# Kernel tuning notes

Hardware: AMD Instinct MI355X
Metric: run time of the kernel (lower is better)

The kernel has to match this reference:

```python
import jax, jax.numpy as jnp
import numpy as np

N = 20000
E = 640000


def setup_inputs() -> dict:
    key = jax.random.key(0)
    k1, k2, k3, k4 = jax.random.split(key, 4)
    IN, H, C = 4096, 512, 10
    x = jax.random.normal(k1, (N, IN), dtype=jnp.float32)
    edge_index = jax.random.randint(k2, (2, E), 0, N, dtype=jnp.int64)
    W1 = jax.random.normal(k3, (IN, H), dtype=jnp.float32) * (1.0 / np.sqrt(IN))
    b1 = jnp.zeros((H,), dtype=jnp.float32)
    W2 = jax.random.normal(k4, (H, C), dtype=jnp.float32) * (1.0 / np.sqrt(H))
    b2 = jnp.zeros((C,), dtype=jnp.float32)
    return {"x": x, "edge_index": edge_index, "W1": W1, "b1": b1, "W2": W2, "b2": b2}


def _gcn_conv(x, src, dst, W, b):
    # Dense transform first (PyG GCNConv does XW then propagate).
    h = x @ W  # [N, F_out]
    # Add self loops.
    loops = jnp.arange(N, dtype=src.dtype)
    s = jnp.concatenate([src, loops])
    d = jnp.concatenate([dst, loops])
    # Symmetric normalization D^{-1/2} (A+I) D^{-1/2}; degree counted on dst.
    deg = jax.ops.segment_sum(jnp.ones_like(d, dtype=h.dtype), d, num_segments=N)
    dinv = jnp.where(deg > 0, jax.lax.rsqrt(deg), 0.0)
    norm = dinv[s] * dinv[d]  # [E+N]
    msg = h[s] * norm[:, None]  # gather + scale
    out = jax.ops.segment_sum(msg, d, num_segments=N)  # scatter-add aggregate
    return out + b


def reference(x, edge_index, W1, b1, W2, b2):
    src, dst = edge_index[0], edge_index[1]
    h = _gcn_conv(x, src, dst, W1, b1)  # conv1 (dropout disabled / eval)
    h = jax.nn.relu(h)
    h = _gcn_conv(h, src, dst, W2, b2)  # conv2
    return jax.nn.log_softmax(h, axis=1)
```

## Files before the change

kernel.cpp:

```cpp
#include <hip/hip_runtime.h>
#include <cstdint>
#include <cstddef>

#define NN  20000
#define EE  640000
#define KIN 4096
#define HD  512
#define NC  10
#define CAP 128

typedef __attribute__((ext_vector_type(8))) short short8;
typedef __attribute__((ext_vector_type(4))) float f32x4;

__device__ __forceinline__ unsigned short f2b(float f) {
  union { float f; unsigned int u; } v; v.f = f;
  unsigned int r = v.u + 0x7fffu + ((v.u >> 16) & 1u);
  return (unsigned short)(r >> 16);
}

__device__ __forceinline__ void gload16(const void* g, void* l) {
  __builtin_amdgcn_global_load_lds(
      (const __attribute__((address_space(1))) unsigned int*)g,
      (__attribute__((address_space(3))) unsigned int*)l, 16, 0, 0);
}

__global__ __launch_bounds__(256) void scatk(const int* __restrict__ src, const int* __restrict__ dst,
                                             int* __restrict__ deg, int* __restrict__ csr) {
  int e = blockIdx.x * 256 + threadIdx.x;
  if (e < EE) {
    int d = dst[e];
    int p = atomicAdd(&deg[d], 1);
    csr[d * CAP + p] = src[e];
  }
}

__global__ __launch_bounds__(256) void dinvk(const int* __restrict__ deg, float* __restrict__ dinv) {
  int i = blockIdx.x * 256 + threadIdx.x;
  if (i < NN) dinv[i] = 1.0f / sqrtf((float)(deg[i] + 1));
}

__global__ __launch_bounds__(256) void transk(const float* __restrict__ W1, unsigned short* __restrict__ w1t) {
  __shared__ float tile[32][33];
  int h0 = blockIdx.x * 32;
  int k0 = blockIdx.y * 32;
  int tx = threadIdx.x & 31, ty = threadIdx.x >> 5;
#pragma unroll
  for (int r = 0; r < 4; ++r) {
    int k = ty * 4 + r;
    tile[k][tx] = W1[(size_t)(k0 + k) * HD + h0 + tx];
  }
  __syncthreads();
#pragma unroll
  for (int r = 0; r < 4; ++r) {
    int h = ty * 4 + r;
    w1t[(size_t)(h0 + h) * KIN + k0 + tx] = f2b(tile[tx][h]);
  }
}

__global__ __launch_bounds__(256) void gemm1(const float* __restrict__ x,
                                             const unsigned short* __restrict__ w1t,
                                             unsigned short* __restrict__ h1b) {
  __shared__ __align__(16) unsigned short As[64 * 64];
  __shared__ __align__(16) unsigned short Bs[128 * 64];
  int t = threadIdx.x;
  int l = t & 63, w = t >> 6;
  int wm = w >> 1, wn = w & 1;
  int bm = (int)(blockIdx.x >> 2) * 64;
  int bn = (int)(blockIdx.x & 3) * 128;

  int stRow = t >> 3;
  int stQ = (t & 7) ^ (stRow & 7);
  const float* ga[2];
#pragma unroll
  for (int i = 0; i < 2; ++i) {
    int m = bm + i * 32 + stRow;
    if (m > NN - 1) m = NN - 1;
    ga[i] = x + (size_t)m * KIN + stQ * 8;
  }

  int rl = l >> 3;
  int cq = (l & 7) ^ rl;
  const unsigned short* gb[4];
  unsigned short* lB[4];
#pragma unroll
  for (int i = 0; i < 4; ++i) {
    int rowB = bn + i * 32 + w * 8 + rl;
    gb[i] = w1t + (size_t)rowB * KIN + cq * 8;
    lB[i] = Bs + (i * 32 + w * 8) * 64;
  }

  int col0 = ((l >> 4) ^ (l & 7));
  int fm[2], fn[4];
#pragma unroll
  for (int i = 0; i < 2; ++i) fm[i] = (wm * 32 + i * 16 + (l & 15)) * 64 + col0 * 8;
#pragma unroll
  for (int j = 0; j < 4; ++j) fn[j] = (wn * 64 + j * 16 + (l & 15)) * 64 + col0 * 8;

  f32x4 acc[2][4] = {};

  for (int kt = 0; kt < KIN / 64; ++kt) {
    int k0 = kt * 64;
    __syncthreads();
#pragma unroll
    for (int i = 0; i < 4; ++i) gload16(gb[i] + k0, lB[i]);
#pragma unroll
    for (int i = 0; i < 2; ++i) {
      float4 a0 = *reinterpret_cast<const float4*>(ga[i] + k0);
      float4 a1 = *reinterpret_cast<const float4*>(ga[i] + k0 + 4);
      uint4 val;
      val.x = (unsigned int)f2b(a0.x) | ((unsigned int)f2b(a0.y) << 16);
      val.y = (unsigned int)f2b(a0.z) | ((unsigned int)f2b(a0.w) << 16);
      val.z = (unsigned int)f2b(a1.x) | ((unsigned int)f2b(a1.y) << 16);
      val.w = (unsigned int)f2b(a1.z) | ((unsigned int)f2b(a1.w) << 16);
      *reinterpret_cast<uint4*>(As + i * 2048 + 8 * t) = val;
    }
    __syncthreads();
#pragma unroll
    for (int kk = 0; kk < 2; ++kk) {
      int xr = kk << 5;
      short8 af[2], bf[4];
#pragma unroll
      for (int i = 0; i < 2; ++i) af[i] = *reinterpret_cast<const short8*>(As + (fm[i] ^ xr));
#pragma unroll
      for (int j = 0; j < 4; ++j) bf[j] = *reinterpret_cast<const short8*>(Bs + (fn[j] ^ xr));
#pragma unroll
      for (int i = 0; i < 2; ++i)
#pragma unroll
        for (int j = 0; j < 4; ++j)
          acc[i][j] = __builtin_amdgcn_mfma_f32_16x16x32_bf16(af[i], bf[j], acc[i][j], 0, 0, 0);
    }
  }

  int lq = l >> 4;
  bool even = (l & 1) == 0;
#pragma unroll
  for (int i = 0; i < 2; ++i) {
    int row0 = bm + wm * 32 + i * 16 + lq * 4;
#pragma unroll
    for (int j = 0; j < 4; ++j) {
      int col = bn + wn * 64 + j * 16 + (l & 15);
#pragma unroll
      for (int r = 0; r < 4; ++r) {
        float v0 = acc[i][j][r];
        float v1 = __shfl_xor(v0, 1);
        int row = row0 + r;
        if (even && row < NN) {
          unsigned int pk = (unsigned int)f2b(v0) | ((unsigned int)f2b(v1) << 16);
          *reinterpret_cast<unsigned int*>(h1b + (size_t)row * HD + col) = pk;
        }
      }
    }
  }
}

__global__ __launch_bounds__(256) void sgk(const unsigned short* __restrict__ h1b, const int* __restrict__ deg,
                                           const int* __restrict__ csr, const float* __restrict__ dinv,
                                           const float* __restrict__ b1, const float* __restrict__ W2,
                                           float* __restrict__ h2) {
  __shared__ int s_idx[CAP];
  __shared__ float s_w[CAP];
  __shared__ float red[4][NC];
  int i = blockIdx.x;
  int c = threadIdx.x;
  float di = dinv[i];
  int dg = deg[i];
  if (c < dg) {
    int s = csr[i * CAP + c];
    s_idx[c] = s;
    s_w[c] = dinv[s] * di;
  }
  const unsigned int* h1v = reinterpret_cast<const unsigned int*>(h1b);
  unsigned int su = h1v[(size_t)i * 256 + c];
  float wself = di * di;
  float a0 = __uint_as_float(su << 16) * wself;
  float a1 = __uint_as_float(su & 0xffff0000u) * wself;
  __syncthreads();
#pragma unroll 4
  for (int jj = 0; jj < dg; ++jj) {
    unsigned int u = h1v[(size_t)s_idx[jj] * 256 + c];
    float wgt = s_w[jj];
    a0 += __uint_as_float(u << 16) * wgt;
    a1 += __uint_as_float(u & 0xffff0000u) * wgt;
  }
  float2 bb = reinterpret_cast<const float2*>(b1)[c];
  float zx = fmaxf(a0 + bb.x, 0.f);
  float zy = fmaxf(a1 + bb.y, 0.f);
  const float* w2r = W2 + (size_t)(2 * c) * NC;
  float part[NC];
#pragma unroll
  for (int cc = 0; cc < NC; ++cc) part[cc] = zx * w2r[cc] + zy * w2r[NC + cc];
#pragma unroll
  for (int cc = 0; cc < NC; ++cc) {
#pragma unroll
    for (int m = 1; m < 64; m <<= 1) part[cc] += __shfl_xor(part[cc], m, 64);
  }
  int wv = c >> 6, ln = c & 63;
  if (ln == 0) {
#pragma unroll
    for (int cc = 0; cc < NC; ++cc) red[wv][cc] = part[cc];
  }
  __syncthreads();
  if (c < NC) h2[(size_t)i * NC + c] = red[0][c] + red[1][c] + red[2][c] + red[3][c];
}

__global__ __launch_bounds__(64) void spmm2(const float* __restrict__ h2, const int* __restrict__ deg,
                                            const int* __restrict__ csr, const float* __restrict__ dinv,
                                            const float* __restrict__ b2, float* __restrict__ out) {
  int i = blockIdx.x;
  int l = threadIdx.x;
  float di = dinv[i];
  int dg = deg[i];
  float acc[NC] = {};
  for (int e = l; e < dg; e += 64) {
    int s = csr[i * CAP + e];
    float wgt = dinv[s] * di;
    const float2* hp = reinterpret_cast<const float2*>(h2 + (size_t)s * NC);
#pragma unroll
    for (int cc = 0; cc < 5; ++cc) {
      float2 v = hp[cc];
      acc[2 * cc] += v.x * wgt;
      acc[2 * cc + 1] += v.y * wgt;
    }
  }
  if (l == 0) {
    float ws = di * di;
#pragma unroll
    for (int cc = 0; cc < NC; ++cc) acc[cc] += h2[(size_t)i * NC + cc] * ws;
  }
#pragma unroll
  for (int cc = 0; cc < NC; ++cc) {
#pragma unroll
    for (int m = 1; m < 64; m <<= 1) acc[cc] += __shfl_xor(acc[cc], m, 64);
  }
  if (l == 0) {
    float v[NC];
    float mx = -1e30f;
#pragma unroll
    for (int cc = 0; cc < NC; ++cc) {
      v[cc] = acc[cc] + b2[cc];
      mx = fmaxf(mx, v[cc]);
    }
    float s = 0.f;
#pragma unroll
    for (int cc = 0; cc < NC; ++cc) s += expf(v[cc] - mx);
    float lse = mx + logf(s);
#pragma unroll
    for (int cc = 0; cc < NC; ++cc) out[(size_t)i * NC + cc] = v[cc] - lse;
  }
}

extern "C" void kernel_launch(void* const* d_in, const int* in_sizes, int n_in,
                              void* d_out, int out_size, void* d_ws, size_t ws_size,
                              hipStream_t stream) {
  (void)in_sizes; (void)n_in; (void)out_size; (void)ws_size;
  const float* x  = (const float*)d_in[0];
  const int*   ei = (const int*)d_in[1];
  const float* W1 = (const float*)d_in[2];
  const float* b1 = (const float*)d_in[3];
  const float* W2 = (const float*)d_in[4];
  const float* b2 = (const float*)d_in[5];
  float* out = (float*)d_out;
  char* ws = (char*)d_ws;

  unsigned short* w1t = (unsigned short*)(ws);
  unsigned short* h1b = (unsigned short*)(ws + 4194304);
  float* h2   = (float*)(ws + 24674304);
  int*   deg  = (int*)(ws + 25474304);
  float* dinv = (float*)(ws + 25554304);
  int*   csr  = (int*)(ws + 25634304);

  const int* srcp = ei;
  const int* dstp = ei + EE;

  hipMemsetAsync(deg, 0, NN * sizeof(int), stream);
  scatk<<<(EE + 255) / 256, 256, 0, stream>>>(srcp, dstp, deg, csr);
  dinvk<<<(NN + 255) / 256, 256, 0, stream>>>(deg, dinv);
  transk<<<dim3(16, 128), 256, 0, stream>>>(W1, w1t);
  gemm1<<<313 * 4, 256, 0, stream>>>(x, w1t, h1b);
  sgk<<<NN, 256, 0, stream>>>(h1b, deg, csr, dinv, b1, W2, h2);
  spmm2<<<NN, 64, 0, stream>>>(h2, deg, csr, dinv, b2, out);
}
```

Baseline: 740.3 us.

## Remap GEMM blocks across XCDs, use packed bf16 convert, widen aggregation loads

Three separate changes. gemm1 block indices are remapped so each group of 8 interleaved blocks covers a contiguous range of tiles. The aim is for neighbouring tiles to land on the same XCD and share L2 for the x rows and W1 columns; the grid is padded to 1256 blocks so it divides by 8. The software bf16 rounding is replaced with the hardware v_cvt_pk_bf16_f32 instruction. The sgk aggregation kernel now uses 128 threads that each gather 4 bf16 features with a uint2 load, which halves the thread count and the wave-reduction partials. The risks are the changed tile order, lower occupancy per block in sgk, and possible NaN-handling differences in the conversion.

```diff
diff --git a/kernel.cpp b/kernel.cpp
--- a/kernel.cpp
+++ b/kernel.cpp
@@ -18,11 +18,20 @@
   return (unsigned short)(r >> 16);
 }
 
+__device__ __forceinline__ unsigned int cvt2(float lo, float hi) {
+  unsigned int r;
+  asm("v_cvt_pk_bf16_f32 %0, %1, %2" : "=v"(r) : "v"(lo), "v"(hi));
+  return r;
+}
+
 __device__ __forceinline__ void gload16(const void* g, void* l) {
   __builtin_amdgcn_global_load_lds(
       (const __attribute__((address_space(1))) unsigned int*)g,
       (__attribute__((address_space(3))) unsigned int*)l, 16, 0, 0);
 }
+
+__device__ __forceinline__ float bflo(unsigned int u) { return __uint_as_float(u << 16); }
+__device__ __forceinline__ float bfhi(unsigned int u) { return __uint_as_float(u & 0xffff0000u); }
 
 __global__ __launch_bounds__(256) void scatk(const int* __restrict__ src, const int* __restrict__ dst,
                                              int* __restrict__ deg, int* __restrict__ csr) {
@@ -65,8 +74,11 @@
   int t = threadIdx.x;
   int l = t & 63, w = t >> 6;
   int wm = w >> 1, wn = w & 1;
-  int bm = (int)(blockIdx.x >> 2) * 64;
-  int bn = (int)(blockIdx.x & 3) * 128;
+
+  int orig = blockIdx.x;
+  int g = (orig & 7) * 157 + (orig >> 3);
+  int bm = (g >> 2) * 64;
+  int bn = (g & 3) * 128;
 
   int stRow = t >> 3;
   int stQ = (t & 7) ^ (stRow & 7);
@@ -108,10 +120,10 @@
       float4 a0 = *reinterpret_cast<const float4*>(ga[i] + k0);
       float4 a1 = *reinterpret_cast<const float4*>(ga[i] + k0 + 4);
       uint4 val;
-      val.x = (unsigned int)f2b(a0.x) | ((unsigned int)f2b(a0.y) << 16);
-      val.y = (unsigned int)f2b(a0.z) | ((unsigned int)f2b(a0.w) << 16);
-      val.z = (unsigned int)f2b(a1.x) | ((unsigned int)f2b(a1.y) << 16);
-      val.w = (unsigned int)f2b(a1.z) | ((unsigned int)f2b(a1.w) << 16);
+      val.x = cvt2(a0.x, a0.y);
+      val.y = cvt2(a0.z, a0.w);
+      val.z = cvt2(a1.x, a1.y);
+      val.w = cvt2(a1.z, a1.w);
       *reinterpret_cast<uint4*>(As + i * 2048 + 8 * t) = val;
     }
     __syncthreads();
@@ -145,21 +157,20 @@
         float v1 = __shfl_xor(v0, 1);
         int row = row0 + r;
         if (even && row < NN) {
-          unsigned int pk = (unsigned int)f2b(v0) | ((unsigned int)f2b(v1) << 16);
-          *reinterpret_cast<unsigned int*>(h1b + (size_t)row * HD + col) = pk;
+          *reinterpret_cast<unsigned int*>(h1b + (size_t)row * HD + col) = cvt2(v0, v1);
         }
       }
     }
   }
 }
 
-__global__ __launch_bounds__(256) void sgk(const unsigned short* __restrict__ h1b, const int* __restrict__ deg,
+__global__ __launch_bounds__(128) void sgk(const unsigned short* __restrict__ h1b, const int* __restrict__ deg,
                                            const int* __restrict__ csr, const float* __restrict__ dinv,
                                            const float* __restrict__ b1, const float* __restrict__ W2,
                                            float* __restrict__ h2) {
   __shared__ int s_idx[CAP];
   __shared__ float s_w[CAP];
-  __shared__ float red[4][NC];
+  __shared__ float red[2][NC];
   int i = blockIdx.x;
   int c = threadIdx.x;
   float di = dinv[i];
@@ -169,26 +180,31 @@
     s_idx[c] = s;
     s_w[c] = dinv[s] * di;
   }
-  const unsigned int* h1v = reinterpret_cast<const unsigned int*>(h1b);
-  unsigned int su = h1v[(size_t)i * 256 + c];
+  const uint2* h1v = reinterpret_cast<const uint2*>(h1b);
+  uint2 su = h1v[(size_t)i * 128 + c];
   float wself = di * di;
-  float a0 = __uint_as_float(su << 16) * wself;
-  float a1 = __uint_as_float(su & 0xffff0000u) * wself;
+  float a0 = bflo(su.x) * wself, a1 = bfhi(su.x) * wself;
+  float a2 = bflo(su.y) * wself, a3 = bfhi(su.y) * wself;
   __syncthreads();
 #pragma unroll 4
   for (int jj = 0; jj < dg; ++jj) {
-    unsigned int u = h1v[(size_t)s_idx[jj] * 256 + c];
+    uint2 u = h1v[(size_t)s_idx[jj] * 128 + c];
     float wgt = s_w[jj];
-    a0 += __uint_as_float(u << 16) * wgt;
-    a1 += __uint_as_float(u & 0xffff0000u) * wgt;
-  }
-  float2 bb = reinterpret_cast<const float2*>(b1)[c];
-  float zx = fmaxf(a0 + bb.x, 0.f);
-  float zy = fmaxf(a1 + bb.y, 0.f);
-  const float* w2r = W2 + (size_t)(2 * c) * NC;
+    a0 += bflo(u.x) * wgt;
+    a1 += bfhi(u.x) * wgt;
+    a2 += bflo(u.y) * wgt;
+    a3 += bfhi(u.y) * wgt;
+  }
+  float4 bb = reinterpret_cast<const float4*>(b1)[c];
+  float z0 = fmaxf(a0 + bb.x, 0.f);
+  float z1 = fmaxf(a1 + bb.y, 0.f);
+  float z2 = fmaxf(a2 + bb.z, 0.f);
+  float z3 = fmaxf(a3 + bb.w, 0.f);
+  const float* w2r = W2 + (size_t)(4 * c) * NC;
   float part[NC];
 #pragma unroll
-  for (int cc = 0; cc < NC; ++cc) part[cc] = zx * w2r[cc] + zy * w2r[NC + cc];
+  for (int cc = 0; cc < NC; ++cc)
+    part[cc] = z0 * w2r[cc] + z1 * w2r[NC + cc] + z2 * w2r[2 * NC + cc] + z3 * w2r[3 * NC + cc];
 #pragma unroll
   for (int cc = 0; cc < NC; ++cc) {
 #pragma unroll
@@ -200,7 +216,7 @@
     for (int cc = 0; cc < NC; ++cc) red[wv][cc] = part[cc];
   }
   __syncthreads();
-  if (c < NC) h2[(size_t)i * NC + c] = red[0][c] + red[1][c] + red[2][c] + red[3][c];
+  if (c < NC) h2[(size_t)i * NC + c] = red[0][c] + red[1][c];
 }
 
 __global__ __launch_bounds__(64) void spmm2(const float* __restrict__ h2, const int* __restrict__ deg,
@@ -276,7 +292,7 @@
   scatk<<<(EE + 255) / 256, 256, 0, stream>>>(srcp, dstp, deg, csr);
   dinvk<<<(NN + 255) / 256, 256, 0, stream>>>(deg, dinv);
   transk<<<dim3(16, 128), 256, 0, stream>>>(W1, w1t);
-  gemm1<<<313 * 4, 256, 0, stream>>>(x, w1t, h1b);
-  sgk<<<NN, 256, 0, stream>>>(h1b, deg, csr, dinv, b1, W2, h2);
+  gemm1<<<314 * 4, 256, 0, stream>>>(x, w1t, h1b);
+  sgk<<<NN, 128, 0, stream>>>(h1b, deg, csr, dinv, b1, W2, h2);
   spmm2<<<NN, 64, 0, stream>>>(h2, deg, csr, dinv, b2, out);
 }
```

After: 666.8 us. -9.9%, faster.
